# Performance work log

Hardware: AMD Instinct MI355X
Metric: run time of the kernel (lower is better)

## Reference

```python
import jax, jax.numpy as jnp
import numpy as np
from jax import lax

TAU = 30.0  # softmax temperature


def setup_inputs() -> dict:
    key = jax.random.key(0)
    ks = jax.random.split(key, 6)
    N, Ci, Co, H, K, KW = 16, 64, 64, 256, 3, 4
    x = jax.random.normal(ks[0], (N, Ci, H, H), jnp.float32)
    # bank of KW candidate kernels: (Co, KW, Ci, K, K), kaiming-ish scale
    w_bank = jax.random.normal(ks[1], (Co, KW, Ci, K, K), jnp.float32) * (2.0 / (Co * K * K)) ** 0.5
    b_bank = jax.random.normal(ks[2], (Co, KW), jnp.float32) * 0.01
    # attention MLP (two 1x1 convs): Ci -> Ci//KW -> KW
    att_w1 = jax.random.normal(ks[3], (Ci // KW, Ci), jnp.float32) * (1.0 / Ci) ** 0.5
    att_b1 = jnp.zeros((Ci // KW,), jnp.float32)
    att_w2 = jax.random.normal(ks[4], (KW, Ci // KW), jnp.float32) * (KW / Ci) ** 0.5
    att_b2 = jnp.zeros((KW,), jnp.float32)
    return {"x": x, "w_bank": w_bank, "b_bank": b_bank,
            "att_w1": att_w1, "att_b1": att_b1, "att_w2": att_w2, "att_b2": att_b2}


def reference(x, w_bank, b_bank, att_w1, att_b1, att_w2, att_b2):
    # attention over weight banks: 1x1 conv -> ReLU -> 1x1 conv -> global avg pool -> softmax(/tau)
    h = jax.nn.relu(jnp.einsum('nchw,dc->ndhw', x, att_w1) + att_b1[None, :, None, None])
    logits = jnp.einsum('ndhw,ed->nehw', h, att_w2) + att_b2[None, :, None, None]
    pooled = jnp.mean(logits, axis=(2, 3))          # [N, KW] (avg_pool2d with kernel=H on square input)
    pi = jax.nn.softmax(pooled / TAU, axis=1)       # [N, KW]
    # per-sample aggregated kernels/biases
    w = jnp.einsum('okcij,nk->nocij', w_bank, pi)   # [N, Co, Ci, K, K]
    b = jnp.einsum('ok,nk->no', b_bank, pi)         # [N, Co]
    # per-sample conv (equivalent to the groups=N conv2d trick)
    def conv_one(xi, wi):
        return lax.conv_general_dilated(xi[None], wi, window_strides=(1, 1),
                                        padding=[(1, 1), (1, 1)],
                                        dimension_numbers=('NCHW', 'OIHW', 'NCHW'))[0]
    y = jax.vmap(conv_one)(x, w)                    # [N, Co, H, W]
    return y + b[:, :, None, None]
```

## Files before the change

kernel.cpp:

```cpp
#include <hip/hip_runtime.h>
#include <hip/hip_bf16.h>

typedef short short8 __attribute__((ext_vector_type(8)));
typedef float f32x4 __attribute__((ext_vector_type(4)));
typedef unsigned short ushort_t;

#define AS1 __attribute__((address_space(1)))
#define AS3 __attribute__((address_space(3)))

__device__ __forceinline__ ushort_t f2bf(float f) {
    unsigned u = __builtin_bit_cast(unsigned, f);
    unsigned r = (u + 0x7FFFu + ((u >> 16) & 1u)) >> 16;
    return (ushort_t)r;
}

__device__ __forceinline__ void gload_lds16(const void* g, void* l) {
    __builtin_amdgcn_global_load_lds((const AS1 unsigned*)g, (AS3 unsigned*)l, 16, 0, 0);
}

__global__ __launch_bounds__(256) void dc_k1_stage_attn(
    const float* __restrict__ x, const float* __restrict__ w1,
    const float* __restrict__ b1, float* __restrict__ s_glob,
    ushort_t* __restrict__ x_t)
{
    __shared__ unsigned xt32[256 * 32];
    __shared__ ushort_t w1s[16 * 64];
    __shared__ float sacc[16];

    const int n = blockIdx.y, h = blockIdx.x, t = threadIdx.x;

    if (h == 0 || h == 255) {
        const int row = (h == 0) ? 0 : 257;
        short8 z = {0, 0, 0, 0, 0, 0, 0, 0};
        short8* p = reinterpret_cast<short8*>(x_t + (size_t)(n * 258 + row) * 258 * 64);
        for (int i = t; i < 2064; i += 256) p[i] = z;
    }

    if (t < 16) sacc[t] = 0.f;
#pragma unroll
    for (int q = 0; q < 4; ++q) { int idx = q * 256 + t; w1s[idx] = f2bf(w1[idx]); }

    const float* xr = x + ((size_t)n * 64) * 65536 + (size_t)h * 256;
    const int sw = (t & 7) << 2;
    for (int cp = 0; cp < 32; ++cp) {
        float a = xr[(size_t)(2 * cp) * 65536 + t];
        float b = xr[(size_t)(2 * cp + 1) * 65536 + t];
        xt32[(t * 32 + cp) ^ sw] = (unsigned)f2bf(a) | ((unsigned)f2bf(b) << 16);
    }
    __syncthreads();

    const int lane = t & 63, wv = t >> 6, l15 = lane & 15, lg = lane >> 4;
    const short8* xt8 = reinterpret_cast<const short8*>(xt32);
    const short8* w18 = reinterpret_cast<const short8*>(w1s);

    short8 a0 = w18[l15 * 8 + lg];
    short8 a1 = w18[l15 * 8 + 4 + lg];
    float b1v[4];
#pragma unroll
    for (int r = 0; r < 4; ++r) b1v[r] = b1[lg * 4 + r];

    float rs[4] = {0.f, 0.f, 0.f, 0.f};
#pragma unroll
    for (int q = 0; q < 4; ++q) {
        int px = (wv * 4 + q) * 16 + l15;
        int pb = px * 8, ps = px & 7;
        short8 bb0 = xt8[pb + (lg ^ ps)];
        short8 bb1 = xt8[pb + ((4 + lg) ^ ps)];
        f32x4 hacc = {0.f, 0.f, 0.f, 0.f};
        hacc = __builtin_amdgcn_mfma_f32_16x16x32_bf16(a0, bb0, hacc, 0, 0, 0);
        hacc = __builtin_amdgcn_mfma_f32_16x16x32_bf16(a1, bb1, hacc, 0, 0, 0);
#pragma unroll
        for (int r = 0; r < 4; ++r) rs[r] += fmaxf(hacc[r] + b1v[r], 0.f);
    }
#pragma unroll
    for (int off = 1; off < 16; off <<= 1)
#pragma unroll
        for (int r = 0; r < 4; ++r) rs[r] += __shfl_xor(rs[r], off);
    if (l15 == 0) {
#pragma unroll
        for (int r = 0; r < 4; ++r) atomicAdd(&sacc[lg * 4 + r], rs[r]);
    }
    __syncthreads();
    if (t < 16) atomicAdd(&s_glob[n * 16 + t], sacc[t]);

    ushort_t* xo = x_t + (((size_t)n * 258 + h + 1) * 258 + 1) * 64;
    const int cb = t & 7, pxr = t >> 3;
#pragma unroll
    for (int rr = 0; rr < 8; ++rr) {
        int px = rr * 32 + pxr;
        short8 v = xt8[px * 8 + (cb ^ (px & 7))];
        *reinterpret_cast<short8*>(xo + (size_t)px * 64 + cb * 8) = v;
    }
    if (t < 16) {
        short8 z = {0, 0, 0, 0, 0, 0, 0, 0};
        size_t colbase = (((size_t)n * 258 + h + 1) * 258 + ((t < 8) ? 0 : 257)) * 64;
        reinterpret_cast<short8*>(x_t + colbase)[t & 7] = z;
    }
}

__global__ void dc_k2_agg(const float* __restrict__ s_glob,
                          const float* __restrict__ w2,
                          const float* __restrict__ b2,
                          const float* __restrict__ b_bank,
                          const float* __restrict__ w_bank,
                          float* __restrict__ b_agg,
                          ushort_t* __restrict__ A_frag)
{
    __shared__ float lw[2304];
    const int o = blockIdx.x, n = blockIdx.y, t = threadIdx.x;

    float z[4];
#pragma unroll
    for (int e = 0; e < 4; ++e) {
        float p = 0.f;
        for (int d = 0; d < 16; ++d) p += w2[e * 16 + d] * s_glob[n * 16 + d];
        z[e] = (b2[e] + p * (1.f / 65536.f)) * (1.f / 30.f);
    }
    float m = fmaxf(fmaxf(z[0], z[1]), fmaxf(z[2], z[3]));
    float ex[4], sum = 0.f;
#pragma unroll
    for (int e = 0; e < 4; ++e) { ex[e] = expf(z[e] - m); sum += ex[e]; }
    float inv = 1.f / sum;
    const float p0 = ex[0] * inv, p1 = ex[1] * inv, p2 = ex[2] * inv, p3 = ex[3] * inv;

    const float* wrow = w_bank + (size_t)o * 2304;
    for (int rr = 0; rr < 36; ++rr) lw[rr * 64 + t] = wrow[rr * 64 + t];
    __syncthreads();

    const int c = t;
    const int cc = c >> 5, lg = (c >> 3) & 3, e = c & 7;
    const int mf = o >> 4, l15 = o & 15;
    ushort_t* base = A_frag + (size_t)n * 18 * 4 * 64 * 8;
#pragma unroll
    for (int ij = 0; ij < 9; ++ij) {
        float v = p0 * lw[0 * 576 + c * 9 + ij] + p1 * lw[1 * 576 + c * 9 + ij]
                + p2 * lw[2 * 576 + c * 9 + ij] + p3 * lw[3 * 576 + c * 9 + ij];
        int ks = ij * 2 + cc;
        base[(((ks * 4 + mf) * 64) + (lg * 16 + l15)) * 8 + e] = f2bf(v);
    }
    if (t == 0)
        b_agg[n * 64 + o] = p0 * b_bank[o * 4 + 0] + p1 * b_bank[o * 4 + 1]
                          + p2 * b_bank[o * 4 + 2] + p3 * b_bank[o * 4 + 3];
}

__global__ __launch_bounds__(512, 1) void dc_k3_conv(
    const ushort_t* __restrict__ x_t, const ushort_t* __restrict__ A_frag,
    const float* __restrict__ b_agg, float* __restrict__ out)
{
    __shared__ char lds[49152 + 6 * 17408];
    char* ldsA = lds;
    char* ldsW = lds + 49152;

    int bid = blockIdx.x;
    int nb = (bid & 7) * 32 + (bid >> 3);
    const int n = nb >> 4;
    const int half = nb & 1;
    const int strip = (nb >> 1) & 7;
    const int h0 = strip * 32;
    const int w0 = half << 7;

    const int t = threadIdx.x, lane = t & 63, wv = t >> 6;
    const int l15 = lane & 15, lg = lane >> 4;
    const int pxl = wv * 16;

    const char* srcb = (const char*)x_t;
    const char* Asrc = (const char*)A_frag + (size_t)n * 73728;

    auto stage_row = [&](int rr, int slot) {
        size_t rowoff = ((size_t)(n * 258 + h0 + rr) * 258 + w0) * 128;
        char* dst = ldsW + slot * 17408;
        for (int k = wv; k < 17; k += 8) {
            unsigned q = k * 1024 + lane * 16;
            unsigned so = q ^ (((q >> 7) & 7) << 4);
            gload_lds16(srcb + rowoff + so, dst + k * 1024);
        }
    };

    for (int q = 0; q < 6; ++q) {
        int jc = wv * 6 + q;
        int gj = (jc < 24) ? jc : jc + 24;
        gload_lds16(Asrc + gj * 1024 + lane * 16, ldsA + jc * 1024);
    }
    short8 aki1[6][4];
#pragma unroll
    for (int s = 0; s < 6; ++s)
#pragma unroll
        for (int mf = 0; mf < 4; ++mf)
            aki1[s][mf] = *reinterpret_cast<const short8*>(
                Asrc + ((6 + s) * 4 + mf) * 1024 + lane * 16);
    for (int r = 0; r < 6; ++r) stage_row(r, r);
    asm volatile("s_waitcnt vmcnt(0)" ::: "memory");
    __builtin_amdgcn_s_barrier();
    __builtin_amdgcn_sched_barrier(0);

    int boff[3][2];
#pragma unroll
    for (int kj = 0; kj < 3; ++kj)
#pragma unroll
        for (int cc = 0; cc < 2; ++cc) {
            int colL = pxl + l15 + kj;
            boff[kj][cc] = (colL * 128 + cc * 64 + lg * 16)
                           ^ ((colL & 7) << 4);
        }
    const int aoff = lane * 16;

    const float* bn = b_agg + n * 64;
    float bv[4][4];
#pragma unroll
    for (int mf = 0; mf < 4; ++mf)
#pragma unroll
        for (int r = 0; r < 4; ++r) bv[mf][r] = bn[mf * 16 + lg * 4 + r];

#pragma unroll 1
    for (int j = 0; j < 16; ++j) {
        const int r0 = 2 * j;
        const int r6 = r0 + 6, r7 = r0 + 7;

        const char* sb[4] = { ldsW + (r0 % 6) * 17408,
                              ldsW + ((r0 + 1) % 6) * 17408,
                              ldsW + ((r0 + 2) % 6) * 17408,
                              ldsW + ((r0 + 3) % 6) * 17408 };

        f32x4 acc[4][2] = {};
        short8 afb[2][4], bfb[2][2];

#pragma unroll
        for (int mf = 0; mf < 4; ++mf)
            afb[0][mf] = *reinterpret_cast<const short8*>(ldsA + mf * 1024 + aoff);
#pragma unroll
        for (int o = 0; o < 2; ++o)
            bfb[0][o] = *reinterpret_cast<const short8*>(sb[o] + boff[0][0]);
#pragma unroll
        for (int s = 0; s < 6; ++s) {
            const int cur = s & 1, nxt = cur ^ 1;
            if (s < 5) {
                const int k1 = s + 1;
#pragma unroll
                for (int mf = 0; mf < 4; ++mf)
                    afb[nxt][mf] = *reinterpret_cast<const short8*>(
                        ldsA + k1 * 4096 + mf * 1024 + aoff);
#pragma unroll
                for (int o = 0; o < 2; ++o)
                    bfb[nxt][o] = *reinterpret_cast<const short8*>(
                        sb[o] + boff[k1 >> 1][k1 & 1]);
            }
            __builtin_amdgcn_s_setprio(1);
#pragma unroll
            for (int mf = 0; mf < 4; ++mf)
#pragma unroll
                for (int o = 0; o < 2; ++o)
                    acc[mf][o] = __builtin_amdgcn_mfma_f32_16x16x32_bf16(
                        afb[cur][mf], bfb[cur][o], acc[mf][o], 0, 0, 0);
            __builtin_amdgcn_s_setprio(0);
        }
        __builtin_amdgcn_s_barrier();
        if (r6 <= 33) stage_row(r6, r0 % 6);
        __builtin_amdgcn_sched_barrier(0);

#pragma unroll
        for (int o = 0; o < 2; ++o)
            bfb[0][o] = *reinterpret_cast<const short8*>(sb[1 + o] + boff[0][0]);
#pragma unroll
        for (int s = 0; s < 6; ++s) {
            const int cur = s & 1, nxt = cur ^ 1;
            if (s < 5) {
                const int k1 = s + 1;
#pragma unroll
                for (int o = 0; o < 2; ++o)
                    bfb[nxt][o] = *reinterpret_cast<const short8*>(
                        sb[1 + o] + boff[k1 >> 1][k1 & 1]);
            }
            __builtin_amdgcn_s_setprio(1);
#pragma unroll
            for (int mf = 0; mf < 4; ++mf)
#pragma unroll
                for (int o = 0; o < 2; ++o)
                    acc[mf][o] = __builtin_amdgcn_mfma_f32_16x16x32_bf16(
                        aki1[s][mf], bfb[cur][o], acc[mf][o], 0, 0, 0);
            __builtin_amdgcn_s_setprio(0);
        }
        __builtin_amdgcn_s_barrier();
        if (r7 <= 33) stage_row(r7, (r0 + 1) % 6);
        __builtin_amdgcn_sched_barrier(0);

#pragma unroll
        for (int mf = 0; mf < 4; ++mf)
            afb[0][mf] = *reinterpret_cast<const short8*>(
                ldsA + 6 * 4096 + mf * 1024 + aoff);
#pragma unroll
        for (int o = 0; o < 2; ++o)
            bfb[0][o] = *reinterpret_cast<const short8*>(sb[2 + o] + boff[0][0]);
#pragma unroll
        for (int s = 0; s < 6; ++s) {
            const int cur = s & 1, nxt = cur ^ 1;
            if (s < 5) {
                const int k1 = s + 1;
#pragma unroll
                for (int mf = 0; mf < 4; ++mf)
                    afb[nxt][mf] = *reinterpret_cast<const short8*>(
                        ldsA + (6 + k1) * 4096 + mf * 1024 + aoff);
#pragma unroll
                for (int o = 0; o < 2; ++o)
                    bfb[nxt][o] = *reinterpret_cast<const short8*>(
                        sb[2 + o] + boff[k1 >> 1][k1 & 1]);
            }
            __builtin_amdgcn_s_setprio(1);
#pragma unroll
            for (int mf = 0; mf < 4; ++mf)
#pragma unroll
                for (int o = 0; o < 2; ++o)
                    acc[mf][o] = __builtin_amdgcn_mfma_f32_16x16x32_bf16(
                        afb[cur][mf], bfb[cur][o], acc[mf][o], 0, 0, 0);
            __builtin_amdgcn_s_setprio(0);
        }

#pragma unroll
        for (int o = 0; o < 2; ++o) {
            const int h = h0 + r0 + o;
#pragma unroll
            for (int mf = 0; mf < 4; ++mf) {
                const int col = w0 + pxl + l15;
#pragma unroll
                for (int r = 0; r < 4; ++r)
                    out[((size_t)(n * 64 + mf * 16 + lg * 4 + r) << 16)
                        + (size_t)h * 256 + col] = acc[mf][o][r] + bv[mf][r];
            }
        }
        __builtin_amdgcn_sched_barrier(0);
        asm volatile("s_waitcnt vmcnt(38)" ::: "memory");
        __builtin_amdgcn_s_barrier();
        __builtin_amdgcn_sched_barrier(0);
    }
}

extern "C" void kernel_launch(void* const* d_in, const int* in_sizes, int n_in,
                              void* d_out, int out_size, void* d_ws, size_t ws_size,
                              hipStream_t stream) {
    const float* x      = (const float*)d_in[0];
    const float* w_bank = (const float*)d_in[1];
    const float* b_bank = (const float*)d_in[2];
    const float* att_w1 = (const float*)d_in[3];
    const float* att_b1 = (const float*)d_in[4];
    const float* att_w2 = (const float*)d_in[5];
    const float* att_b2 = (const float*)d_in[6];
    float* out = (float*)d_out;

    char* ws = (char*)d_ws;
    float*    s_glob = (float*)ws;
    float*    b_agg  = (float*)(ws + 2048);
    ushort_t* A_frag = (ushort_t*)(ws + 8192);
    ushort_t* x_t    = (ushort_t*)(ws + (2ull << 20));

    hipMemsetAsync(s_glob, 0, 16 * 16 * sizeof(float), stream);

    dc_k1_stage_attn<<<dim3(256, 16), 256, 0, stream>>>(x, att_w1, att_b1, s_glob, x_t);
    dc_k2_agg<<<dim3(64, 16), 64, 0, stream>>>(s_glob, att_w2, att_b2, b_bank,
                                               w_bank, b_agg, A_frag);
    dc_k3_conv<<<256, 512, 0, stream>>>(x_t, A_frag, b_agg, out);
}
```

Baseline: 191.9 us.

## Retile conv into 64-column quarter tiles with register-resident weights, two blocks per CU

The conv kernel now uses 256-thread blocks over 64-column quarter tiles (512 blocks) instead of 512-thread blocks over half rows. Each wave holds its 32-output-channel half of all 18 weight k-steps in registers, so the LDS weight staging and per-step A-fragment LDS reads go away. Each wave computes a 32x32 output tile per row pair, which gives more MFMA per B-fragment load. LDS drops to about 54KB so two blocks can share a CU for latency hiding. The cost is heavier register pressure from 36 short8 weight fragments plus 8 accumulators, which may cause spills, and some input columns at tile edges are staged twice.

```diff
diff --git a/kernel.cpp b/kernel.cpp
--- a/kernel.cpp
+++ b/kernel.cpp
@@ -143,188 +143,139 @@
                           + p2 * b_bank[o * 4 + 2] + p3 * b_bank[o * 4 + 3];
 }
 
-__global__ __launch_bounds__(512, 1) void dc_k3_conv(
+__global__ __launch_bounds__(256, 2) void dc_k3_conv(
     const ushort_t* __restrict__ x_t, const ushort_t* __restrict__ A_frag,
     const float* __restrict__ b_agg, float* __restrict__ out)
 {
-    __shared__ char lds[49152 + 6 * 17408];
-    char* ldsA = lds;
-    char* ldsW = lds + 49152;
+    __shared__ char ldsW[6 * 9216];
 
     int bid = blockIdx.x;
-    int nb = (bid & 7) * 32 + (bid >> 3);
-    const int n = nb >> 4;
-    const int half = nb & 1;
-    const int strip = (nb >> 1) & 7;
+    int nb = (bid & 7) * 64 + (bid >> 3);
+    const int n = nb >> 5;
+    const int tile = nb & 31;
+    const int strip = tile >> 2;
+    const int quarter = tile & 3;
     const int h0 = strip * 32;
-    const int w0 = half << 7;
+    const int c0 = quarter * 64;
 
     const int t = threadIdx.x, lane = t & 63, wv = t >> 6;
     const int l15 = lane & 15, lg = lane >> 4;
-    const int pxl = wv * 16;
+    const int mh = wv & 1;
+    const int pxl = (wv >> 1) * 32;
 
     const char* srcb = (const char*)x_t;
     const char* Asrc = (const char*)A_frag + (size_t)n * 73728;
 
     auto stage_row = [&](int rr, int slot) {
-        size_t rowoff = ((size_t)(n * 258 + h0 + rr) * 258 + w0) * 128;
-        char* dst = ldsW + slot * 17408;
-        for (int k = wv; k < 17; k += 8) {
+        size_t rowoff = ((size_t)(n * 258 + h0 + rr) * 258 + c0) * 128;
+        char* dst = ldsW + slot * 9216;
+        for (int k = wv; k < 9; k += 4) {
             unsigned q = k * 1024 + lane * 16;
             unsigned so = q ^ (((q >> 7) & 7) << 4);
             gload_lds16(srcb + rowoff + so, dst + k * 1024);
         }
     };
 
-    for (int q = 0; q < 6; ++q) {
-        int jc = wv * 6 + q;
-        int gj = (jc < 24) ? jc : jc + 24;
-        gload_lds16(Asrc + gj * 1024 + lane * 16, ldsA + jc * 1024);
-    }
-    short8 aki1[6][4];
-#pragma unroll
-    for (int s = 0; s < 6; ++s)
-#pragma unroll
-        for (int mf = 0; mf < 4; ++mf)
-            aki1[s][mf] = *reinterpret_cast<const short8*>(
-                Asrc + ((6 + s) * 4 + mf) * 1024 + lane * 16);
+    short8 aki[18][2];
+#pragma unroll
+    for (int ks = 0; ks < 18; ++ks)
+#pragma unroll
+        for (int m = 0; m < 2; ++m)
+            aki[ks][m] = *reinterpret_cast<const short8*>(
+                Asrc + (size_t)(ks * 4 + mh * 2 + m) * 1024 + lane * 16);
     for (int r = 0; r < 6; ++r) stage_row(r, r);
     asm volatile("s_waitcnt vmcnt(0)" ::: "memory");
     __builtin_amdgcn_s_barrier();
     __builtin_amdgcn_sched_barrier(0);
 
-    int boff[3][2];
+    int boff[3][2][2];
 #pragma unroll
     for (int kj = 0; kj < 3; ++kj)
 #pragma unroll
-        for (int cc = 0; cc < 2; ++cc) {
-            int colL = pxl + l15 + kj;
-            boff[kj][cc] = (colL * 128 + cc * 64 + lg * 16)
-                           ^ ((colL & 7) << 4);
-        }
-    const int aoff = lane * 16;
+        for (int cc = 0; cc < 2; ++cc)
+#pragma unroll
+            for (int nf = 0; nf < 2; ++nf) {
+                int colL = pxl + nf * 16 + l15 + kj;
+                boff[kj][cc][nf] = (colL * 128 + cc * 64 + lg * 16)
+                                   ^ ((colL & 7) << 4);
+            }
 
     const float* bn = b_agg + n * 64;
-    float bv[4][4];
-#pragma unroll
-    for (int mf = 0; mf < 4; ++mf)
-#pragma unroll
-        for (int r = 0; r < 4; ++r) bv[mf][r] = bn[mf * 16 + lg * 4 + r];
+    float bv[2][4];
+#pragma unroll
+    for (int m = 0; m < 2; ++m)
+#pragma unroll
+        for (int r = 0; r < 4; ++r) bv[m][r] = bn[mh * 32 + m * 16 + lg * 4 + r];
 
 #pragma unroll 1
     for (int j = 0; j < 16; ++j) {
         const int r0 = 2 * j;
         const int r6 = r0 + 6, r7 = r0 + 7;
 
-        const char* sb[4] = { ldsW + (r0 % 6) * 17408,
-                              ldsW + ((r0 + 1) % 6) * 17408,
-                              ldsW + ((r0 + 2) % 6) * 17408,
-                              ldsW + ((r0 + 3) % 6) * 17408 };
-
-        f32x4 acc[4][2] = {};
-        short8 afb[2][4], bfb[2][2];
-
-#pragma unroll
-        for (int mf = 0; mf < 4; ++mf)
-            afb[0][mf] = *reinterpret_cast<const short8*>(ldsA + mf * 1024 + aoff);
-#pragma unroll
-        for (int o = 0; o < 2; ++o)
-            bfb[0][o] = *reinterpret_cast<const short8*>(sb[o] + boff[0][0]);
-#pragma unroll
-        for (int s = 0; s < 6; ++s) {
-            const int cur = s & 1, nxt = cur ^ 1;
-            if (s < 5) {
-                const int k1 = s + 1;
-#pragma unroll
-                for (int mf = 0; mf < 4; ++mf)
-                    afb[nxt][mf] = *reinterpret_cast<const short8*>(
-                        ldsA + k1 * 4096 + mf * 1024 + aoff);
-#pragma unroll
-                for (int o = 0; o < 2; ++o)
-                    bfb[nxt][o] = *reinterpret_cast<const short8*>(
-                        sb[o] + boff[k1 >> 1][k1 & 1]);
+        const char* sb[4] = { ldsW + (r0 % 6) * 9216,
+                              ldsW + ((r0 + 1) % 6) * 9216,
+                              ldsW + ((r0 + 2) % 6) * 9216,
+                              ldsW + ((r0 + 3) % 6) * 9216 };
+
+        f32x4 acc[2][2][2] = {};
+        short8 bfb[2][2][2];
+
+#pragma unroll
+        for (int ki = 0; ki < 3; ++ki) {
+#pragma unroll
+            for (int o = 0; o < 2; ++o)
+#pragma unroll
+                for (int nf = 0; nf < 2; ++nf)
+                    bfb[0][o][nf] = *reinterpret_cast<const short8*>(
+                        sb[ki + o] + boff[0][0][nf]);
+#pragma unroll
+            for (int s = 0; s < 6; ++s) {
+                const int cur = s & 1, nxt = cur ^ 1;
+                if (s < 5) {
+                    const int k1 = s + 1;
+#pragma unroll
+                    for (int o = 0; o < 2; ++o)
+#pragma unroll
+                        for (int nf = 0; nf < 2; ++nf)
+                            bfb[nxt][o][nf] = *reinterpret_cast<const short8*>(
+                                sb[ki + o] + boff[k1 >> 1][k1 & 1][nf]);
+                }
+                __builtin_amdgcn_s_setprio(1);
+#pragma unroll
+                for (int m = 0; m < 2; ++m)
+#pragma unroll
+                    for (int nf = 0; nf < 2; ++nf)
+#pragma unroll
+                        for (int o = 0; o < 2; ++o)
+                            acc[m][nf][o] = __builtin_amdgcn_mfma_f32_16x16x32_bf16(
+                                aki[ki * 6 + s][m], bfb[cur][o][nf],
+                                acc[m][nf][o], 0, 0, 0);
+                __builtin_amdgcn_s_setprio(0);
             }
-            __builtin_amdgcn_s_setprio(1);
-#pragma unroll
-            for (int mf = 0; mf < 4; ++mf)
-#pragma unroll
-                for (int o = 0; o < 2; ++o)
-                    acc[mf][o] = __builtin_amdgcn_mfma_f32_16x16x32_bf16(
-                        afb[cur][mf], bfb[cur][o], acc[mf][o], 0, 0, 0);
-            __builtin_amdgcn_s_setprio(0);
-        }
-        __builtin_amdgcn_s_barrier();
-        if (r6 <= 33) stage_row(r6, r0 % 6);
-        __builtin_amdgcn_sched_barrier(0);
-
-#pragma unroll
-        for (int o = 0; o < 2; ++o)
-            bfb[0][o] = *reinterpret_cast<const short8*>(sb[1 + o] + boff[0][0]);
-#pragma unroll
-        for (int s = 0; s < 6; ++s) {
-            const int cur = s & 1, nxt = cur ^ 1;
-            if (s < 5) {
-                const int k1 = s + 1;
-#pragma unroll
-                for (int o = 0; o < 2; ++o)
-                    bfb[nxt][o] = *reinterpret_cast<const short8*>(
-                        sb[1 + o] + boff[k1 >> 1][k1 & 1]);
+            if (ki == 0) {
+                __builtin_amdgcn_s_barrier();
+                if (r6 <= 33) stage_row(r6, r0 % 6);
+                __builtin_amdgcn_sched_barrier(0);
+            } else if (ki == 1) {
+                __builtin_amdgcn_s_barrier();
+                if (r7 <= 33) stage_row(r7, (r0 + 1) % 6);
+                __builtin_amdgcn_sched_barrier(0);
             }
-            __builtin_amdgcn_s_setprio(1);
-#pragma unroll
-            for (int mf = 0; mf < 4; ++mf)
-#pragma unroll
-                for (int o = 0; o < 2; ++o)
-                    acc[mf][o] = __builtin_amdgcn_mfma_f32_16x16x32_bf16(
-                        aki1[s][mf], bfb[cur][o], acc[mf][o], 0, 0, 0);
-            __builtin_amdgcn_s_setprio(0);
-        }
-        __builtin_amdgcn_s_barrier();
-        if (r7 <= 33) stage_row(r7, (r0 + 1) % 6);
-        __builtin_amdgcn_sched_barrier(0);
-
-#pragma unroll
-        for (int mf = 0; mf < 4; ++mf)
-            afb[0][mf] = *reinterpret_cast<const short8*>(
-                ldsA + 6 * 4096 + mf * 1024 + aoff);
-#pragma unroll
-        for (int o = 0; o < 2; ++o)
-            bfb[0][o] = *reinterpret_cast<const short8*>(sb[2 + o] + boff[0][0]);
-#pragma unroll
-        for (int s = 0; s < 6; ++s) {
-            const int cur = s & 1, nxt = cur ^ 1;
-            if (s < 5) {
-                const int k1 = s + 1;
-#pragma unroll
-                for (int mf = 0; mf < 4; ++mf)
-                    afb[nxt][mf] = *reinterpret_cast<const short8*>(
-                        ldsA + (6 + k1) * 4096 + mf * 1024 + aoff);
-#pragma unroll
-                for (int o = 0; o < 2; ++o)
-                    bfb[nxt][o] = *reinterpret_cast<const short8*>(
-                        sb[2 + o] + boff[k1 >> 1][k1 & 1]);
-            }
-            __builtin_amdgcn_s_setprio(1);
-#pragma unroll
-            for (int mf = 0; mf < 4; ++mf)
-#pragma unroll
-                for (int o = 0; o < 2; ++o)
-                    acc[mf][o] = __builtin_amdgcn_mfma_f32_16x16x32_bf16(
-                        afb[cur][mf], bfb[cur][o], acc[mf][o], 0, 0, 0);
-            __builtin_amdgcn_s_setprio(0);
         }
 
 #pragma unroll
         for (int o = 0; o < 2; ++o) {
             const int h = h0 + r0 + o;
 #pragma unroll
-            for (int mf = 0; mf < 4; ++mf) {
-                const int col = w0 + pxl + l15;
-#pragma unroll
-                for (int r = 0; r < 4; ++r)
-                    out[((size_t)(n * 64 + mf * 16 + lg * 4 + r) << 16)
-                        + (size_t)h * 256 + col] = acc[mf][o][r] + bv[mf][r];
-            }
+            for (int m = 0; m < 2; ++m)
+#pragma unroll
+                for (int nf = 0; nf < 2; ++nf) {
+                    const int col = c0 + pxl + nf * 16 + l15;
+#pragma unroll
+                    for (int r = 0; r < 4; ++r)
+                        out[((size_t)(n * 64 + mh * 32 + m * 16 + lg * 4 + r) << 16)
+                            + (size_t)h * 256 + col] = acc[m][nf][o][r] + bv[m][r];
+                }
         }
         __builtin_amdgcn_sched_barrier(0);
         asm volatile("s_waitcnt vmcnt(38)" ::: "memory");
@@ -356,5 +307,5 @@
     dc_k1_stage_attn<<<dim3(256, 16), 256, 0, stream>>>(x, att_w1, att_b1, s_glob, x_t);
     dc_k2_agg<<<dim3(64, 16), 64, 0, stream>>>(s_glob, att_w2, att_b2, b_bank,
                                                w_bank, b_agg, A_frag);
-    dc_k3_conv<<<256, 512, 0, stream>>>(x_t, A_frag, b_agg, out);
-}
+    dc_k3_conv<<<512, 256, 0, stream>>>(x_t, A_frag, b_agg, out);
+}
```

Result: slower. 216.8 us (+13.0%).
